# Optimization experiments

Hardware: AMD Instinct MI355X
Metric: run time of the kernel (lower is better)

Reference implementation:

```python
import jax, jax.numpy as jnp
import numpy as np

F_DIM = 128
N_RBF = 20
CUTOFF = 5.0
N_LAYERS = 3
EPS = 1e-8


def setup_inputs() -> dict:
    key = jax.random.key(0)
    ks = jax.random.split(key, 16)
    N, E = 10000, 320000
    atomic_numbers = jax.random.randint(ks[0], (N,), 0, 100)
    r_ij = jax.random.normal(ks[1], (E, 3), dtype=jnp.float32)
    idx_i = jnp.sort(jax.random.randint(ks[2], (E,), 0, N))
    idx_j = jax.random.randint(ks[3], (E,), 0, N)
    emb = jax.random.normal(ks[4], (100, F_DIM), dtype=jnp.float32)
    emb = emb.at[0].set(0.0)  # padding_idx=0
    s = 0.05
    return {
        "atomic_numbers": atomic_numbers,
        "r_ij": r_ij,
        "idx_i": idx_i,
        "idx_j": idx_j,
        "embedding": emb,
        "filt_W": jax.random.normal(ks[5], (N_RBF, N_LAYERS * 3 * F_DIM), dtype=jnp.float32) * s,
        "filt_b": jax.random.normal(ks[6], (N_LAYERS * 3 * F_DIM,), dtype=jnp.float32) * s,
        "int_W1": jax.random.normal(ks[7], (N_LAYERS, F_DIM, F_DIM), dtype=jnp.float32) * s,
        "int_b1": jax.random.normal(ks[8], (N_LAYERS, F_DIM), dtype=jnp.float32) * s,
        "int_W2": jax.random.normal(ks[9], (N_LAYERS, F_DIM, 3 * F_DIM), dtype=jnp.float32) * s,
        "int_b2": jax.random.normal(ks[10], (N_LAYERS, 3 * F_DIM), dtype=jnp.float32) * s,
        "mix_W1": jax.random.normal(ks[11], (N_LAYERS, 2 * F_DIM, F_DIM), dtype=jnp.float32) * s,
        "mix_b1": jax.random.normal(ks[12], (N_LAYERS, F_DIM), dtype=jnp.float32) * s,
        "mix_W2": jax.random.normal(ks[13], (N_LAYERS, F_DIM, 3 * F_DIM), dtype=jnp.float32) * s,
        "mix_b2": jax.random.normal(ks[14], (N_LAYERS, 3 * F_DIM), dtype=jnp.float32) * s,
        "mux_W": jax.random.normal(ks[15], (N_LAYERS, F_DIM, 2 * F_DIM), dtype=jnp.float32) * s,
    }


def _painn(embedding, filt_W, filt_b, int_W1, int_b1, int_W2, int_b2,
           mix_W1, mix_b1, mix_W2, mix_b2, mux_W,
           r_ij, atomic_numbers, idx_i, idx_j):
    N = atomic_numbers.shape[0]
    F = F_DIM
    d_ij = jnp.linalg.norm(r_ij, axis=1, keepdims=True)          # [E,1]
    dir_ij = r_ij / d_ij                                          # [E,3]
    # Gaussian RBF expansion
    offset = jnp.linspace(0.0, CUTOFF, N_RBF, dtype=jnp.float32)
    coeff = -0.5 / (offset[1] - offset[0]) ** 2
    phi = jnp.exp(coeff * (d_ij[..., None] - offset) ** 2)        # [E,1,n_rbf]
    # Cosine cutoff
    fcut = 0.5 * (jnp.cos(d_ij * jnp.pi / CUTOFF) + 1.0) * (d_ij < CUTOFF)  # [E,1]
    filters = (phi @ filt_W + filt_b) * fcut[..., None]           # [E,1,L*3F]
    filter_list = jnp.split(filters, N_LAYERS, axis=-1)

    q = embedding[atomic_numbers][:, None, :]                     # [N,1,F]
    mu = jnp.zeros((N, 3, F), dtype=q.dtype)

    for i in range(N_LAYERS):
        Wij = filter_list[i]                                      # [E,1,3F]
        # interaction
        h = jax.nn.silu(q @ int_W1[i] + int_b1[i])
        x = h @ int_W2[i] + int_b2[i]                             # [N,1,3F]
        xj = x[idx_j]                                             # [E,1,3F]
        muj = mu[idx_j]                                           # [E,3,F]
        xw = Wij * xj
        dq, dmuR, dmumu = jnp.split(xw, 3, axis=-1)               # each [E,1,F]
        dq = jax.ops.segment_sum(dq, idx_i, num_segments=N)       # [N,1,F]
        dmu = dmuR * dir_ij[:, :, None] + dmumu * muj             # [E,3,F]
        dmu = jax.ops.segment_sum(dmu, idx_i, num_segments=N)     # [N,3,F]
        q = q + dq
        mu = mu + dmu
        # mixing
        mu_mix = mu @ mux_W[i]                                    # [N,3,2F]
        mu_V, mu_W = jnp.split(mu_mix, 2, axis=-1)
        mu_Vn = jnp.sqrt(jnp.sum(mu_V ** 2, axis=-2, keepdims=True) + EPS)  # [N,1,F]
        ctx = jnp.concatenate([q, mu_Vn], axis=-1)                # [N,1,2F]
        h = jax.nn.silu(ctx @ mix_W1[i] + mix_b1[i])
        x = h @ mix_W2[i] + mix_b2[i]                             # [N,1,3F]
        dq_i, dmu_i, dqmu_i = jnp.split(x, 3, axis=-1)
        dmu_i = dmu_i * mu_W                                      # [N,3,F]
        dqmu_i = dqmu_i * jnp.sum(mu_V * mu_W, axis=1, keepdims=True)
        q = q + dq_i + dqmu_i
        mu = mu + dmu_i
    return q[:, 0, :], mu


def reference(atomic_numbers, r_ij, idx_i, idx_j, embedding, filt_W, filt_b,
              int_W1, int_b1, int_W2, int_b2, mix_W1, mix_b1, mix_W2, mix_b2, mux_W):
    return _painn(embedding, filt_W, filt_b, int_W1, int_b1, int_W2, int_b2,
                  mix_W1, mix_b1, mix_W2, mix_b2, mux_W,
                  r_ij, atomic_numbers, idx_i, idx_j)
```

## Files before the change

kernel.cpp:

```cpp
#include <hip/hip_runtime.h>
#include <hip/hip_bf16.h>
#include <hip/hip_fp16.h>

#define F_DIM 128
#define N_RBF 20
#define CUTOFF 5.0f
#define PI_F 3.14159265358979323846f
#define NPB 4

typedef float v2f __attribute__((ext_vector_type(2)));
typedef __attribute__((ext_vector_type(8))) short bf16x8;
typedef __attribute__((ext_vector_type(4))) float f32x4;
typedef _Float16 h2f __attribute__((ext_vector_type(2)));
typedef _Float16 f16x8 __attribute__((ext_vector_type(8)));

__device__ __forceinline__ unsigned int bf16_rtne(float f) {
    unsigned int u = __float_as_uint(f);
    u += 0x7fffu + ((u >> 16) & 1u);
    return u >> 16;
}
__device__ __forceinline__ unsigned int pack_bf2(float lo, float hi) {
    return bf16_rtne(lo) | (bf16_rtne(hi) << 16);
}
__device__ __forceinline__ float unpk_lo(unsigned int u) {
    return __uint_as_float(u << 16);
}
__device__ __forceinline__ float unpk_hi(unsigned int u) {
    return __uint_as_float(u & 0xffff0000u);
}
__device__ __forceinline__ float bf16_to_f(unsigned short s) {
    return __uint_as_float(((unsigned int)s) << 16);
}
__device__ __forceinline__ unsigned int pack_h2(float lo, float hi) {
    h2f h = (h2f){(_Float16)lo, (_Float16)hi};
    return __builtin_bit_cast(unsigned int, h);
}

__global__ __launch_bounds__(256) void k_rowptr(const int* __restrict__ idx_i,
                                                int* __restrict__ row_ptr, int N, int E) {
    int i = blockIdx.x * blockDim.x + threadIdx.x;
    if (i > N) return;
    if (i == N) { row_ptr[N] = E; return; }
    int lo = 0, hi = E;
    while (lo < hi) {
        int mid = (lo + hi) >> 1;
        if (idx_i[mid] < i) lo = mid + 1; else hi = mid;
    }
    row_ptr[i] = lo;
}

__global__ __launch_bounds__(256) void k_init(const int* __restrict__ Z,
                                              const float* __restrict__ emb,
                                              float* __restrict__ q,
                                              unsigned int* __restrict__ P,
                                              float* __restrict__ muD, int N) {
    int idx = blockIdx.x * blockDim.x + threadIdx.x;
    if (idx < N * F_DIM) {
        int n = idx >> 7, f = idx & 127;
        q[idx] = emb[Z[n] * F_DIM + f];
    }
    if (idx < N * 384) { P[idx] = 0u; muD[idx] = 0.f; }
}

__global__ __launch_bounds__(256) void k_prep(const float* __restrict__ muxW,
                                              const float* __restrict__ W1,
                                              const float* __restrict__ W2,
                                              const float* __restrict__ iW1,
                                              const float* __restrict__ iW2,
                                              const float* __restrict__ filt_W,
                                              const float* __restrict__ filt_b,
                                              unsigned short* __restrict__ muxWt,
                                              unsigned short* __restrict__ W1t,
                                              unsigned short* __restrict__ W2t,
                                              unsigned short* __restrict__ iW1t,
                                              unsigned short* __restrict__ iW2t,
                                              unsigned short* __restrict__ filtWt) {
    int idx = blockIdx.x * 256 + threadIdx.x;
    if (idx < 98304) {
        int l = idx / 32768, rem = idx % 32768;
        int c = rem / 128, k = rem % 128;
        muxWt[idx] = (unsigned short)bf16_rtne(muxW[l * 32768 + k * 256 + c]);
    } else if (idx < 196608) {
        int i2 = idx - 98304;
        int l = i2 / 32768, rem = i2 % 32768;
        int c = rem / 256, k = rem % 256;
        W1t[i2] = (unsigned short)bf16_rtne(W1[l * 32768 + k * 128 + c]);
    } else if (idx < 344064) {
        int i2 = idx - 196608;
        int l = i2 / 49152, rem = i2 % 49152;
        int c = rem / 128, k = rem % 128;
        W2t[i2] = (unsigned short)bf16_rtne(W2[l * 49152 + k * 384 + c]);
    } else if (idx < 393216) {
        int i2 = idx - 344064;
        int l = i2 / 16384, rem = i2 % 16384;
        int c = rem / 128, k = rem % 128;
        iW1t[i2] = (unsigned short)bf16_rtne(iW1[l * 16384 + k * 128 + c]);
    } else if (idx < 540672) {
        int i2 = idx - 393216;
        int l = i2 / 49152, rem = i2 % 49152;
        int c = rem / 128, k = rem % 128;
        iW2t[i2] = (unsigned short)bf16_rtne(iW2[l * 49152 + k * 384 + c]);
    } else if (idx < 568320) {
        int i2 = idx - 540672;
        int l = i2 / 9216, rem = i2 % 9216;
        int c = rem / 24, k = rem % 24;
        float v = 0.f;
        if (k < 20)       v = filt_W[k * 1152 + l * 384 + c];
        else if (k == 20) v = filt_b[l * 384 + c];
        _Float16 hv = (_Float16)v;
        filtWt[i2] = __builtin_bit_cast(unsigned short, hv);
    }
}

__global__ __launch_bounds__(256) void k_geom(const float* __restrict__ r,
                                              unsigned int* __restrict__ geom, int E) {
    int e = blockIdx.x * blockDim.x + threadIdx.x;
    if (e >= E) return;
    float x = r[e * 3], y = r[e * 3 + 1], z = r[e * 3 + 2];
    float d = sqrtf(x * x + y * y + z * z);
    float inv = 1.f / d;
    float fc = (d < CUTOFF) ? 0.5f * (__cosf(d * (PI_F / CUTOFF)) + 1.f) : 0.f;
    unsigned int* g = geom + (size_t)e * 16;
    g[0] = __float_as_uint(x * inv);
    g[1] = __float_as_uint(y * inv);
    g[2] = __float_as_uint(z * inv);
    g[3] = __float_as_uint(fc);
    const float delta = CUTOFF / (N_RBF - 1);
    const float coeff = -0.5f / (delta * delta);
    float ph[N_RBF];
#pragma unroll
    for (int k = 0; k < N_RBF; k++) {
        float t = d - k * delta;
        ph[k] = __expf(coeff * t * t) * fc;
    }
#pragma unroll
    for (int k = 0; k < N_RBF / 2; k++)
        g[4 + k] = pack_h2(ph[2 * k], ph[2 * k + 1]);
    g[14] = pack_h2(fc, 0.f);
    g[15] = 0u;
}

__global__ __launch_bounds__(256) void k_node_mfma(
        const float* __restrict__ q,
        const unsigned short* __restrict__ iW1t,
        const float* __restrict__ b1,
        const unsigned short* __restrict__ iW2t,
        const float* __restrict__ b2,
        unsigned int* __restrict__ P, int N) {
    __shared__ unsigned short A[16 * 136];
    __shared__ unsigned short Ah[16 * 136];
    __shared__ float Xs[16 * 396];
    int t = threadIdx.x;
    int w = t >> 6, l = t & 63, quad = l >> 4, c0 = l & 15;
    int n0 = blockIdx.x * 16;

#pragma unroll
    for (int i = 0; i < 4; i++) {
        int flat = i * 256 + t;
        int node = flat >> 6, cp = flat & 63;
        int gn = n0 + node;
        unsigned int v = 0u;
        if (gn < N) { const float* s = q + (size_t)gn * 128 + 2 * cp; v = pack_bf2(s[0], s[1]); }
        *(unsigned int*)&A[node * 136 + 2 * cp] = v;
    }
    __syncthreads();

    bf16x8 a1[4];
#pragma unroll
    for (int ks = 0; ks < 4; ks++)
        a1[ks] = *(const bf16x8*)&A[c0 * 136 + ks * 32 + quad * 8];
#pragma unroll
    for (int jj = 0; jj < 2; jj++) {
        int jg = 2 * w + jj;
        float bb = b1[16 * jg + c0];
        f32x4 acc = (f32x4){bb, bb, bb, bb};
#pragma unroll
        for (int ks = 0; ks < 4; ks++) {
            bf16x8 b = *(const bf16x8*)&iW1t[(16 * jg + c0) * 128 + ks * 32 + quad * 8];
            acc = __builtin_amdgcn_mfma_f32_16x16x32_bf16(a1[ks], b, acc, 0, 0, 0);
        }
#pragma unroll
        for (int r = 0; r < 4; r++) {
            float aa = acc[r];
            Ah[(quad * 4 + r) * 136 + 16 * jg + c0] =
                (unsigned short)bf16_rtne(aa / (1.f + __expf(-aa)));
        }
    }
    __syncthreads();

    bf16x8 a3[4];
#pragma unroll
    for (int ks = 0; ks < 4; ks++)
        a3[ks] = *(const bf16x8*)&Ah[c0 * 136 + ks * 32 + quad * 8];
#pragma unroll
    for (int jj = 0; jj < 6; jj++) {
        int jx = 6 * w + jj;
        float bb = b2[16 * jx + c0];
        f32x4 acc = (f32x4){bb, bb, bb, bb};
#pragma unroll
        for (int ks = 0; ks < 4; ks++) {
            bf16x8 b = *(const bf16x8*)&iW2t[(16 * jx + c0) * 128 + ks * 32 + quad * 8];
            acc = __builtin_amdgcn_mfma_f32_16x16x32_bf16(a3[ks], b, acc, 0, 0, 0);
        }
#pragma unroll
        for (int r = 0; r < 4; r++)
            Xs[(quad * 4 + r) * 396 + 16 * jx + c0] = acc[r];
    }
    __syncthreads();

    int n = t >> 4, fi = (t & 15) * 8;
    int gn = n0 + n;
    if (gn < N) {
        size_t base = (size_t)gn * 384;
        unsigned int d[8];
#pragma unroll
        for (int k = 0; k < 8; k++) {
            float x0 = Xs[n * 396 + fi + k];
            float x1 = Xs[n * 396 + 128 + fi + k];
            float x2 = Xs[n * 396 + 256 + fi + k];
            d[k] = pack_bf2(x0, x1);
            ((unsigned short*)&P[base + 256 + fi + k])[0] = (unsigned short)bf16_rtne(x2);
        }
        *(uint4*)&P[base + fi]     = make_uint4(d[0], d[1], d[2], d[3]);
        *(uint4*)&P[base + fi + 4] = make_uint4(d[4], d[5], d[6], d[7]);
    }
}

__device__ __forceinline__ f16x8 load_phi_frag(const unsigned int* __restrict__ geom,
                                               int ts, int c0, int quad, int E) {
    int ea = ts + c0;
    if (ea >= E) ea = E - 1;
    f16x8 a = {};
    if (quad < 3)
        a = *(const f16x8*)&geom[(size_t)ea * 16 + 4 + quad * 4];
    return a;
}

template <bool HAS_MU>
__global__ __launch_bounds__(256) void k_edge(
        const unsigned int* __restrict__ P,
        const unsigned int* __restrict__ geom,
        const int* __restrict__ idx_j,
        const int* __restrict__ row_ptr,
        const unsigned short* __restrict__ filtWt,
        float* __restrict__ q,
        float* __restrict__ muD, int N, int E) {
    constexpr int NT = HAS_MU ? 6 : 4;
    constexpr int WS = 388;
    __shared__ float Ws[16 * WS];
    __shared__ float red[4][128];
    int t = threadIdx.x;
    int f = t & 127;
    int sub = __builtin_amdgcn_readfirstlane(t >> 7);
    int w = t >> 6, l = t & 63, quad = l >> 4, c0 = l & 15;

    f16x8 Bf[NT];
#pragma unroll
    for (int jj = 0; jj < NT; jj++) {
        int jx = NT * w + jj;
        f16x8 b = {};
        if (quad < 3)
            b = *(const f16x8*)&filtWt[(16 * jx + c0) * 24 + quad * 8];
        Bf[jj] = b;
    }

    int i0 = blockIdx.x * NPB;
    for (int nn = 0; nn < NPB; nn++) {
        int i = i0 + nn;
        if (i >= N) break;
        int rs = __builtin_amdgcn_readfirstlane(row_ptr[i]);
        int re = __builtin_amdgcn_readfirstlane(row_ptr[i + 1]);
        float dq = 0.f;
        v2f dm01 = (v2f){0.f, 0.f};
        float dm2 = 0.f;

        f16x8 a = load_phi_frag(geom, rs, c0, quad, E);
        for (int ts = rs; ts < re; ts += 16) {
#pragma unroll
            for (int jj = 0; jj < NT; jj++) {
                int jx = NT * w + jj;
                f32x4 acc = (f32x4){0.f, 0.f, 0.f, 0.f};
                acc = __builtin_amdgcn_mfma_f32_16x16x32_f16(a, Bf[jj], acc, 0, 0, 0);
#pragma unroll
                for (int r = 0; r < 4; r++)
                    Ws[(quad * 4 + r) * WS + 16 * jx + c0] = acc[r];
            }
            __syncthreads();
            if (ts + 16 < re) a = load_phi_frag(geom, ts + 16, c0, quad, E);

            int te = (re < ts + 16) ? re : ts + 16;
            for (int e = ts + sub; e < te; e += 2) {
                int j = __builtin_amdgcn_readfirstlane(idx_j[e]);
                const unsigned int* Pj = P + (size_t)j * 384;
                unsigned int A = Pj[f];
                unsigned int B = 0, C = 0;
                if (HAS_MU) { B = Pj[128 + f]; C = Pj[256 + f]; }

                const float* g = (const float*)(geom + (size_t)e * 16);
                float dirx = g[0], diry = g[1], dirz = g[2];

                int eloc = e - ts;
                float wq = Ws[eloc * WS + f];
                float wr = Ws[eloc * WS + 128 + f];

                float xq = unpk_lo(A), xr = unpk_hi(A);
                dq += wq * xq;
                float s_r = wr * xr;
                if (HAS_MU) {
                    float wm = Ws[eloc * WS + 256 + f];
                    float xm = unpk_lo(C);
                    float s_m = wm * xm;
                    dm01 += (v2f){s_r, s_r} * (v2f){dirx, diry} +
                            (v2f){s_m, s_m} * (v2f){unpk_lo(B), unpk_hi(B)};
                    dm2  += s_r * dirz + s_m * unpk_hi(C);
                } else {
                    dm01 += (v2f){s_r, s_r} * (v2f){dirx, diry};
                    dm2  += s_r * dirz;
                }
            }
            __syncthreads();
        }

        if (sub == 1) { red[0][f] = dq; red[1][f] = dm01.x; red[2][f] = dm01.y; red[3][f] = dm2; }
        __syncthreads();
        if (sub == 0) {
            dq += red[0][f];
            float d0 = dm01.x + red[1][f], d1 = dm01.y + red[2][f];
            dm2 += red[3][f];
            q[(size_t)i * 128 + f] += dq;
            size_t base = (size_t)i * 384;
            if (HAS_MU) {
                muD[base + f]       += d0;
                muD[base + 128 + f] += d1;
                muD[base + 256 + f] += dm2;
            } else {
                muD[base + f]       = d0;
                muD[base + 128 + f] = d1;
                muD[base + 256 + f] = dm2;
            }
        }
        __syncthreads();
    }
}

__global__ __launch_bounds__(256) void k_mix_fused(
        float* __restrict__ q, float* __restrict__ mu,
        const unsigned short* __restrict__ muxWt,
        const unsigned short* __restrict__ W1t,
        const unsigned short* __restrict__ W2t,
        const float* __restrict__ b1,
        const float* __restrict__ b2,
        const unsigned short* __restrict__ niW1t,
        const float* __restrict__ nib1,
        const unsigned short* __restrict__ niW2t,
        const float* __restrict__ nib2,
        int has_node,
        unsigned int* __restrict__ P, int N) {
    __shared__ unsigned short A[16 * 264];
    __shared__ unsigned short Wsp[3 * 16 * 136];
    __shared__ float Xs[16 * 396];
    __shared__ float Ss[16 * 140];
    int t = threadIdx.x;
    int w = t >> 6, l = t & 63, quad = l >> 4, c0 = l & 15;
    int n0 = blockIdx.x * 16;

#pragma unroll
    for (int i = 0; i < 4; i++) {
        int flat = i * 256 + t;
        int node = flat >> 6, cp = flat & 63;
        int gn = n0 + node;
        unsigned int v = 0u;
        if (gn < N) { const float* s = q + (size_t)gn * 128 + 2 * cp; v = pack_bf2(s[0], s[1]); }
        *(unsigned int*)&A[node * 264 + 2 * cp] = v;
    }

    f32x4 vn2[2], S[2];
#pragma unroll
    for (int jj = 0; jj < 2; jj++) { vn2[jj] = (f32x4){0,0,0,0}; S[jj] = (f32x4){0,0,0,0}; }

    for (int c = 0; c < 3; c++) {
#pragma unroll
        for (int i = 0; i < 4; i++) {
            int flat = i * 256 + t;
            int node = flat >> 6, cp = flat & 63;
            int gn = n0 + node;
            unsigned int v = 0u;
            if (gn < N) {
                const float* s = mu + (size_t)gn * 384 + c * 128 + 2 * cp;
                v = pack_bf2(s[0], s[1]);
            }
            *(unsigned int*)&A[node * 264 + 128 + 2 * cp] = v;
        }
        __syncthreads();
        bf16x8 af[4];
#pragma unroll
        for (int ks = 0; ks < 4; ks++)
            af[ks] = *(const bf16x8*)&A[c0 * 264 + 128 + ks * 32 + quad * 8];
#pragma unroll
        for (int jj = 0; jj < 2; jj++) {
            int jv = 2 * w + jj;
            f32x4 V = (f32x4){0,0,0,0}, Wm = (f32x4){0,0,0,0};
#pragma unroll
            for (int ks = 0; ks < 4; ks++) {
                bf16x8 bV = *(const bf16x8*)&muxWt[(16 * jv + c0) * 128 + ks * 32 + quad * 8];
                V = __builtin_amdgcn_mfma_f32_16x16x32_bf16(af[ks], bV, V, 0, 0, 0);
            }
#pragma unroll
            for (int ks = 0; ks < 4; ks++) {
                bf16x8 bW = *(const bf16x8*)&muxWt[(16 * (jv + 8) + c0) * 128 + ks * 32 + quad * 8];
                Wm = __builtin_amdgcn_mfma_f32_16x16x32_bf16(af[ks], bW, Wm, 0, 0, 0);
            }
            vn2[jj] += V * V;
            S[jj]   += V * Wm;
#pragma unroll
            for (int r = 0; r < 4; r++)
                Wsp[c * 2176 + (quad * 4 + r) * 136 + 16 * jv + c0] =
                    (unsigned short)bf16_rtne(Wm[r]);
        }
        __syncthreads();
    }

#pragma unroll
    for (int jj = 0; jj < 2; jj++) {
        int jv = 2 * w + jj;
#pragma unroll
        for (int r = 0; r < 4; r++)
            A[(quad * 4 + r) * 264 + 128 + 16 * jv + c0] =
                (unsigned short)bf16_rtne(sqrtf(vn2[jj][r] + 1e-8f));
    }
    __syncthreads();

    bf16x8 a2[8];
#pragma unroll
    for (int ks = 0; ks < 8; ks++)
        a2[ks] = *(const bf16x8*)&A[c0 * 264 + ks * 32 + quad * 8];
    {
        unsigned short htmp[2][4];
#pragma unroll
        for (int jj = 0; jj < 2; jj++) {
            int jg = 2 * w + jj;
            float bb = b1[16 * jg + c0];
            f32x4 acc = (f32x4){bb, bb, bb, bb};
#pragma unroll
            for (int ks = 0; ks < 8; ks++) {
                bf16x8 b = *(const bf16x8*)&W1t[(16 * jg + c0) * 256 + ks * 32 + quad * 8];
                acc = __builtin_amdgcn_mfma_f32_16x16x32_bf16(a2[ks], b, acc, 0, 0, 0);
            }
#pragma unroll
            for (int r = 0; r < 4; r++) {
                float aa = acc[r];
                htmp[jj][r] = (unsigned short)bf16_rtne(aa / (1.f + __expf(-aa)));
            }
        }
        __syncthreads();
#pragma unroll
        for (int jj = 0; jj < 2; jj++) {
            int jg = 2 * w + jj;
#pragma unroll
            for (int r = 0; r < 4; r++)
                A[(quad * 4 + r) * 264 + 128 + 16 * jg + c0] = htmp[jj][r];
        }
    }
    __syncthreads();

    bf16x8 a3[4];
#pragma unroll
    for (int ks = 0; ks < 4; ks++)
        a3[ks] = *(const bf16x8*)&A[c0 * 264 + 128 + ks * 32 + quad * 8];
#pragma unroll
    for (int jj = 0; jj < 6; jj++) {
        int jx = 6 * w + jj;
        float bb = b2[16 * jx + c0];
        f32x4 acc = (f32x4){bb, bb, bb, bb};
#pragma unroll
        for (int ks = 0; ks < 4; ks++) {
            bf16x8 b = *(const bf16x8*)&W2t[(16 * jx + c0) * 128 + ks * 32 + quad * 8];
            acc = __builtin_amdgcn_mfma_f32_16x16x32_bf16(a3[ks], b, acc, 0, 0, 0);
        }
#pragma unroll
        for (int r = 0; r < 4; r++)
            Xs[(quad * 4 + r) * 396 + 16 * jx + c0] = acc[r];
    }
#pragma unroll
    for (int jj = 0; jj < 2; jj++) {
        int jv = 2 * w + jj;
#pragma unroll
        for (int r = 0; r < 4; r++)
            Ss[(quad * 4 + r) * 140 + 16 * jv + c0] = S[jj][r];
    }
    __syncthreads();

    int n = t >> 4, fi = (t & 15) * 8;
    int gn = n0 + n;
    if (gn < N) {
        float* qp = q + (size_t)gn * 128 + fi;
        float qn[8];
#pragma unroll
        for (int k = 0; k < 8; k++) {
            qn[k] = qp[k] + Xs[n * 396 + fi + k] +
                    Xs[n * 396 + 256 + fi + k] * Ss[n * 140 + fi + k];
            qp[k] = qn[k];
        }
        unsigned int qd[4];
#pragma unroll
        for (int p = 0; p < 4; p++) qd[p] = pack_bf2(qn[2 * p], qn[2 * p + 1]);
        *(uint4*)&A[n * 264 + fi] = make_uint4(qd[0], qd[1], qd[2], qd[3]);

        size_t base = (size_t)gn * 384;
        float m[3][8];
#pragma unroll
        for (int c = 0; c < 3; c++) {
            float* mp = mu + base + c * 128 + fi;
#pragma unroll
            for (int k = 0; k < 8; k++) {
                m[c][k] = mp[k] + Xs[n * 396 + 128 + fi + k] *
                                  bf16_to_f(Wsp[c * 2176 + n * 136 + fi + k]);
                mp[k] = m[c][k];
            }
        }
        unsigned int d[8];
#pragma unroll
        for (int k = 0; k < 8; k++) {
            d[k] = pack_bf2(m[0][k], m[1][k]);
            ((unsigned short*)&P[base + 256 + fi + k])[1] = (unsigned short)bf16_rtne(m[2][k]);
        }
        *(uint4*)&P[base + 128 + fi]     = make_uint4(d[0], d[1], d[2], d[3]);
        *(uint4*)&P[base + 128 + fi + 4] = make_uint4(d[4], d[5], d[6], d[7]);
    }
    __syncthreads();

    if (has_node) {
        unsigned short* Ah = Wsp;
        bf16x8 a1[4];
#pragma unroll
        for (int ks = 0; ks < 4; ks++)
            a1[ks] = *(const bf16x8*)&A[c0 * 264 + ks * 32 + quad * 8];
#pragma unroll
        for (int jj = 0; jj < 2; jj++) {
            int jg = 2 * w + jj;
            float bb = nib1[16 * jg + c0];
            f32x4 acc = (f32x4){bb, bb, bb, bb};
#pragma unroll
            for (int ks = 0; ks < 4; ks++) {
                bf16x8 b = *(const bf16x8*)&niW1t[(16 * jg + c0) * 128 + ks * 32 + quad * 8];
                acc = __builtin_amdgcn_mfma_f32_16x16x32_bf16(a1[ks], b, acc, 0, 0, 0);
            }
#pragma unroll
            for (int r = 0; r < 4; r++) {
                float aa = acc[r];
                Ah[(quad * 4 + r) * 136 + 16 * jg + c0] =
                    (unsigned short)bf16_rtne(aa / (1.f + __expf(-aa)));
            }
        }
        __syncthreads();

        bf16x8 a4[4];
#pragma unroll
        for (int ks = 0; ks < 4; ks++)
            a4[ks] = *(const bf16x8*)&Ah[c0 * 136 + ks * 32 + quad * 8];
#pragma unroll
        for (int jj = 0; jj < 6; jj++) {
            int jx = 6 * w + jj;
            float bb = nib2[16 * jx + c0];
            f32x4 acc = (f32x4){bb, bb, bb, bb};
#pragma unroll
            for (int ks = 0; ks < 4; ks++) {
                bf16x8 b = *(const bf16x8*)&niW2t[(16 * jx + c0) * 128 + ks * 32 + quad * 8];
                acc = __builtin_amdgcn_mfma_f32_16x16x32_bf16(a4[ks], b, acc, 0, 0, 0);
            }
#pragma unroll
            for (int r = 0; r < 4; r++)
                Xs[(quad * 4 + r) * 396 + 16 * jx + c0] = acc[r];
        }
        __syncthreads();

        if (gn < N) {
            size_t base = (size_t)gn * 384;
            unsigned int d[8];
#pragma unroll
            for (int k = 0; k < 8; k++) {
                float x0 = Xs[n * 396 + fi + k];
                float x1 = Xs[n * 396 + 128 + fi + k];
                float x2 = Xs[n * 396 + 256 + fi + k];
                d[k] = pack_bf2(x0, x1);
                ((unsigned short*)&P[base + 256 + fi + k])[0] = (unsigned short)bf16_rtne(x2);
            }
            *(uint4*)&P[base + fi]     = make_uint4(d[0], d[1], d[2], d[3]);
            *(uint4*)&P[base + fi + 4] = make_uint4(d[4], d[5], d[6], d[7]);
        }
    }
}

extern "C" void kernel_launch(void* const* d_in, const int* in_sizes, int n_in,
                              void* d_out, int out_size, void* d_ws, size_t ws_size,
                              hipStream_t stream) {
    const int*   Z      = (const int*)d_in[0];
    const float* r_ij   = (const float*)d_in[1];
    const int*   idx_i  = (const int*)d_in[2];
    const int*   idx_j  = (const int*)d_in[3];
    const float* emb    = (const float*)d_in[4];
    const float* filt_W = (const float*)d_in[5];
    const float* filt_b = (const float*)d_in[6];
    const float* int_W1 = (const float*)d_in[7];
    const float* int_b1 = (const float*)d_in[8];
    const float* int_W2 = (const float*)d_in[9];
    const float* int_b2 = (const float*)d_in[10];
    const float* mix_W1 = (const float*)d_in[11];
    const float* mix_b1 = (const float*)d_in[12];
    const float* mix_W2 = (const float*)d_in[13];
    const float* mix_b2 = (const float*)d_in[14];
    const float* mux_W  = (const float*)d_in[15];

    int N = in_sizes[0];
    int E = in_sizes[2];

    float* q   = (float*)d_out;
    float* muD = q + (size_t)N * 128;

    unsigned int* geom = (unsigned int*)d_ws;
    unsigned int* P = geom + (size_t)E * 16;
    int* row_ptr = (int*)(P + (size_t)N * 384);
    uintptr_t waddr = (uintptr_t)(row_ptr + N + 1);
    waddr = (waddr + 15) & ~(uintptr_t)15;
    unsigned short* muxWt = (unsigned short*)waddr;
    unsigned short* W1t   = muxWt + 98304;
    unsigned short* W2t   = W1t + 98304;
    unsigned short* iW1t  = W2t + 147456;
    unsigned short* iW2t  = iW1t + 49152;
    unsigned short* filtWt = iW2t + 147456;

    k_rowptr<<<(N + 1 + 255) / 256, 256, 0, stream>>>(idx_i, row_ptr, N, E);
    k_init<<<((size_t)N * 384 + 255) / 256, 256, 0, stream>>>(Z, emb, q, P, muD, N);
    k_geom<<<(E + 255) / 256, 256, 0, stream>>>(r_ij, geom, E);
    k_prep<<<2220, 256, 0, stream>>>(mux_W, mix_W1, mix_W2, int_W1, int_W2, filt_W, filt_b,
                                     muxWt, W1t, W2t, iW1t, iW2t, filtWt);

    int tiles = (N + 15) / 16;
    k_node_mfma<<<tiles, 256, 0, stream>>>(
        q, iW1t, int_b1, iW2t, int_b2, P, N);
    for (int l = 0; l < 3; l++) {
        if (l == 0)
            k_edge<false><<<(N + NPB - 1) / NPB, 256, 0, stream>>>(
                P, geom, idx_j, row_ptr, filtWt, q, muD, N, E);
        else
            k_edge<true><<<(N + NPB - 1) / NPB, 256, 0, stream>>>(
                P, geom, idx_j, row_ptr, filtWt + (size_t)l * 9216, q, muD, N, E);
        int nl = (l < 2) ? (l + 1) : 0;
        k_mix_fused<<<tiles, 256, 0, stream>>>(
            q, muD, muxWt + (size_t)l * 32768, W1t + (size_t)l * 32768,
            W2t + (size_t)l * 49152, mix_b1 + l * 128, mix_b2 + l * 384,
            iW1t + (size_t)nl * 16384, int_b1 + nl * 128,
            iW2t + (size_t)nl * 49152, int_b2 + nl * 384,
            (l < 2) ? 1 : 0, P, N);
    }
}
```

Before: 539.9 us.

## Software-pipeline neighbor gathers in edge kernel and route directions through MFMA

The edge kernel now prefetches the next tile's idx_j indices, phi fragments and gathered neighbor P rows into registers while the current tile is processed, using a fixed 8-iteration unrolled loop with masking. Edge direction vectors are packed as fp16 into the geometry record and extracted through an extra identity-column MFMA block, so they are read from LDS instead of global memory. Nodes per block drop from 4 to 2 and the reduction buffer reuses the Ws LDS space. This is meant to hide gather latency at the cost of more registers, directions rounded to fp16, and wasted work on masked edges in partial tiles.

```diff
diff --git a/kernel.cpp b/kernel.cpp
--- a/kernel.cpp
+++ b/kernel.cpp
@@ -6,7 +6,7 @@
 #define N_RBF 20
 #define CUTOFF 5.0f
 #define PI_F 3.14159265358979323846f
-#define NPB 4
+#define NPB 2
 
 typedef float v2f __attribute__((ext_vector_type(2)));
 typedef __attribute__((ext_vector_type(8))) short bf16x8;
@@ -100,13 +100,18 @@
         int l = i2 / 49152, rem = i2 % 49152;
         int c = rem / 128, k = rem % 128;
         iW2t[i2] = (unsigned short)bf16_rtne(iW2[l * 49152 + k * 384 + c]);
-    } else if (idx < 568320) {
+    } else if (idx < 569472) {
         int i2 = idx - 540672;
-        int l = i2 / 9216, rem = i2 % 9216;
+        int l = i2 / 9600, rem = i2 % 9600;
         int c = rem / 24, k = rem % 24;
         float v = 0.f;
-        if (k < 20)       v = filt_W[k * 1152 + l * 384 + c];
-        else if (k == 20) v = filt_b[l * 384 + c];
+        if (c < 384) {
+            if (k < 20)       v = filt_W[k * 1152 + l * 384 + c];
+            else if (k == 20) v = filt_b[l * 384 + c];
+        } else {
+            int comp = c - 384;
+            if (comp < 3 && k == 21 + comp) v = 1.f;
+        }
         _Float16 hv = (_Float16)v;
         filtWt[i2] = __builtin_bit_cast(unsigned short, hv);
     }
@@ -121,9 +126,10 @@
     float inv = 1.f / d;
     float fc = (d < CUTOFF) ? 0.5f * (__cosf(d * (PI_F / CUTOFF)) + 1.f) : 0.f;
     unsigned int* g = geom + (size_t)e * 16;
-    g[0] = __float_as_uint(x * inv);
-    g[1] = __float_as_uint(y * inv);
-    g[2] = __float_as_uint(z * inv);
+    float dx = x * inv, dy = y * inv, dz = z * inv;
+    g[0] = __float_as_uint(dx);
+    g[1] = __float_as_uint(dy);
+    g[2] = __float_as_uint(dz);
     g[3] = __float_as_uint(fc);
     const float delta = CUTOFF / (N_RBF - 1);
     const float coeff = -0.5f / (delta * delta);
@@ -136,8 +142,8 @@
 #pragma unroll
     for (int k = 0; k < N_RBF / 2; k++)
         g[4 + k] = pack_h2(ph[2 * k], ph[2 * k + 1]);
-    g[14] = pack_h2(fc, 0.f);
-    g[15] = 0u;
+    g[14] = pack_h2(fc, dx);
+    g[15] = pack_h2(dy, dz);
 }
 
 __global__ __launch_bounds__(256) void k_node_mfma(
@@ -246,12 +252,11 @@
         float* __restrict__ q,
         float* __restrict__ muD, int N, int E) {
     constexpr int NT = HAS_MU ? 6 : 4;
-    constexpr int WS = 388;
+    constexpr int WS = 404;
     __shared__ float Ws[16 * WS];
-    __shared__ float red[4][128];
     int t = threadIdx.x;
     int f = t & 127;
-    int sub = __builtin_amdgcn_readfirstlane(t >> 7);
+    int sub = t >> 7;
     int w = t >> 6, l = t & 63, quad = l >> 4, c0 = l & 15;
 
     f16x8 Bf[NT];
@@ -263,79 +268,114 @@
             b = *(const f16x8*)&filtWt[(16 * jx + c0) * 24 + quad * 8];
         Bf[jj] = b;
     }
+    f16x8 BfX = {};
+    if (w == 3 && quad < 3)
+        BfX = *(const f16x8*)&filtWt[(384 + c0) * 24 + quad * 8];
 
     int i0 = blockIdx.x * NPB;
+    int Rs = __builtin_amdgcn_readfirstlane(row_ptr[i0]);
+
+    unsigned int RA[8], RB[8], RC[8];
+    f16x8 aF = load_phi_frag(geom, Rs, c0, quad, E);
+#pragma unroll
+    for (int k = 0; k < 8; k++) {
+        int e0 = Rs + 2 * k + sub; if (e0 > E - 1) e0 = E - 1;
+        int j = __builtin_amdgcn_readfirstlane(idx_j[e0]);
+        const unsigned int* Pj = P + (size_t)j * 384;
+        RA[k] = Pj[f];
+        if (HAS_MU) { RB[k] = Pj[128 + f]; RC[k] = Pj[256 + f]; }
+    }
+
     for (int nn = 0; nn < NPB; nn++) {
         int i = i0 + nn;
         if (i >= N) break;
         int rs = __builtin_amdgcn_readfirstlane(row_ptr[i]);
         int re = __builtin_amdgcn_readfirstlane(row_ptr[i + 1]);
-        float dq = 0.f;
-        v2f dm01 = (v2f){0.f, 0.f};
-        float dm2 = 0.f;
-
-        f16x8 a = load_phi_frag(geom, rs, c0, quad, E);
+        float dq = 0.f, dm0 = 0.f, dm1 = 0.f, dm2 = 0.f;
+
         for (int ts = rs; ts < re; ts += 16) {
 #pragma unroll
             for (int jj = 0; jj < NT; jj++) {
                 int jx = NT * w + jj;
                 f32x4 acc = (f32x4){0.f, 0.f, 0.f, 0.f};
-                acc = __builtin_amdgcn_mfma_f32_16x16x32_f16(a, Bf[jj], acc, 0, 0, 0);
+                acc = __builtin_amdgcn_mfma_f32_16x16x32_f16(aF, Bf[jj], acc, 0, 0, 0);
 #pragma unroll
                 for (int r = 0; r < 4; r++)
                     Ws[(quad * 4 + r) * WS + 16 * jx + c0] = acc[r];
             }
+            if (w == 3) {
+                f32x4 acc = (f32x4){0.f, 0.f, 0.f, 0.f};
+                acc = __builtin_amdgcn_mfma_f32_16x16x32_f16(aF, BfX, acc, 0, 0, 0);
+#pragma unroll
+                for (int r = 0; r < 4; r++)
+                    Ws[(quad * 4 + r) * WS + 384 + c0] = acc[r];
+            }
+
+            int nts = (ts + 16 < re) ? ts + 16 : re;
+            int RJ[8];
+#pragma unroll
+            for (int k = 0; k < 8; k++) {
+                int en = nts + 2 * k + sub; if (en > E - 1) en = E - 1;
+                RJ[k] = idx_j[en];
+            }
+            f16x8 aN = load_phi_frag(geom, nts, c0, quad, E);
             __syncthreads();
-            if (ts + 16 < re) a = load_phi_frag(geom, ts + 16, c0, quad, E);
-
-            int te = (re < ts + 16) ? re : ts + 16;
-            for (int e = ts + sub; e < te; e += 2) {
-                int j = __builtin_amdgcn_readfirstlane(idx_j[e]);
-                const unsigned int* Pj = P + (size_t)j * 384;
-                unsigned int A = Pj[f];
-                unsigned int B = 0, C = 0;
-                if (HAS_MU) { B = Pj[128 + f]; C = Pj[256 + f]; }
-
-                const float* g = (const float*)(geom + (size_t)e * 16);
-                float dirx = g[0], diry = g[1], dirz = g[2];
-
-                int eloc = e - ts;
-                float wq = Ws[eloc * WS + f];
-                float wr = Ws[eloc * WS + 128 + f];
-
+
+            int nv = re - ts; if (nv > 16) nv = 16;
+#pragma unroll
+            for (int k = 0; k < 8; k++) {
+                int eloc = 2 * k + sub;
+                float msk = (eloc < nv) ? 1.f : 0.f;
+                float wq = Ws[eloc * WS + f] * msk;
+                float wr = Ws[eloc * WS + 128 + f] * msk;
+                float dx = Ws[eloc * WS + 384];
+                float dy = Ws[eloc * WS + 385];
+                float dz = Ws[eloc * WS + 386];
+                unsigned int A = RA[k];
                 float xq = unpk_lo(A), xr = unpk_hi(A);
                 dq += wq * xq;
                 float s_r = wr * xr;
                 if (HAS_MU) {
-                    float wm = Ws[eloc * WS + 256 + f];
-                    float xm = unpk_lo(C);
-                    float s_m = wm * xm;
-                    dm01 += (v2f){s_r, s_r} * (v2f){dirx, diry} +
-                            (v2f){s_m, s_m} * (v2f){unpk_lo(B), unpk_hi(B)};
-                    dm2  += s_r * dirz + s_m * unpk_hi(C);
+                    float wm = Ws[eloc * WS + 256 + f] * msk;
+                    unsigned int B = RB[k], C = RC[k];
+                    float s_m = wm * unpk_lo(C);
+                    dm0 += s_r * dx + s_m * unpk_lo(B);
+                    dm1 += s_r * dy + s_m * unpk_hi(B);
+                    dm2 += s_r * dz + s_m * unpk_hi(C);
                 } else {
-                    dm01 += (v2f){s_r, s_r} * (v2f){dirx, diry};
-                    dm2  += s_r * dirz;
+                    dm0 += s_r * dx;
+                    dm1 += s_r * dy;
+                    dm2 += s_r * dz;
                 }
-            }
+                {
+                    int j = __builtin_amdgcn_readfirstlane(RJ[k]);
+                    const unsigned int* Pj = P + (size_t)j * 384;
+                    RA[k] = Pj[f];
+                    if (HAS_MU) { RB[k] = Pj[128 + f]; RC[k] = Pj[256 + f]; }
+                }
+            }
+            aF = aN;
             __syncthreads();
         }
 
-        if (sub == 1) { red[0][f] = dq; red[1][f] = dm01.x; red[2][f] = dm01.y; red[3][f] = dm2; }
+        if (sub == 1) {
+            Ws[f] = dq; Ws[128 + f] = dm0; Ws[256 + f] = dm1; Ws[384 + f] = dm2;
+        }
         __syncthreads();
         if (sub == 0) {
-            dq += red[0][f];
-            float d0 = dm01.x + red[1][f], d1 = dm01.y + red[2][f];
-            dm2 += red[3][f];
+            dq  += Ws[f];
+            dm0 += Ws[128 + f];
+            dm1 += Ws[256 + f];
+            dm2 += Ws[384 + f];
             q[(size_t)i * 128 + f] += dq;
             size_t base = (size_t)i * 384;
             if (HAS_MU) {
-                muD[base + f]       += d0;
-                muD[base + 128 + f] += d1;
+                muD[base + f]       += dm0;
+                muD[base + 128 + f] += dm1;
                 muD[base + 256 + f] += dm2;
             } else {
-                muD[base + f]       = d0;
-                muD[base + 128 + f] = d1;
+                muD[base + f]       = dm0;
+                muD[base + 128 + f] = dm1;
                 muD[base + 256 + f] = dm2;
             }
         }
@@ -632,7 +672,7 @@
     k_rowptr<<<(N + 1 + 255) / 256, 256, 0, stream>>>(idx_i, row_ptr, N, E);
     k_init<<<((size_t)N * 384 + 255) / 256, 256, 0, stream>>>(Z, emb, q, P, muD, N);
     k_geom<<<(E + 255) / 256, 256, 0, stream>>>(r_ij, geom, E);
-    k_prep<<<2220, 256, 0, stream>>>(mux_W, mix_W1, mix_W2, int_W1, int_W2, filt_W, filt_b,
+    k_prep<<<2225, 256, 0, stream>>>(mux_W, mix_W1, mix_W2, int_W1, int_W2, filt_W, filt_b,
                                      muxWt, W1t, W2t, iW1t, iW2t, filtWt);
 
     int tiles = (N + 15) / 16;
@@ -644,7 +684,7 @@
                 P, geom, idx_j, row_ptr, filtWt, q, muD, N, E);
         else
             k_edge<true><<<(N + NPB - 1) / NPB, 256, 0, stream>>>(
-                P, geom, idx_j, row_ptr, filtWt + (size_t)l * 9216, q, muD, N, E);
+                P, geom, idx_j, row_ptr, filtWt + (size_t)l * 9600, q, muD, N, E);
         int nl = (l < 2) ? (l + 1) : 0;
         k_mix_fused<<<tiles, 256, 0, stream>>>(
             q, muD, muxWt + (size_t)l * 32768, W1t + (size_t)l * 32768,
```

New measurement: 568.8 us. 5.4% more time.
